# Performance work log

Hardware: AMD Instinct MI355X
Metric: run time of the kernel (lower is better)

## Reference

```python
import jax, jax.numpy as jnp
import numpy as np

N_NODES = 100000
IN_C = 512
HID = 64   # 2 * out_channels
OUT_C = 32
N_EDGES = 2000000  # knn k=20


def gcn_conv(x, src, dst, W, b, n_nodes):
    """PyG GCNConv: symmetric norm with self-loops. Aggregates src -> dst."""
    h = x @ W  # [N, F_out] -- transform first (F_out small)
    ones = jnp.ones(src.shape[0], dtype=h.dtype)
    deg = jax.ops.segment_sum(ones, dst, num_segments=n_nodes) + 1.0  # +1 self-loop
    dinv = jax.lax.rsqrt(deg)  # deg > 0 always due to self-loop
    norm = dinv[src] * dinv[dst]                      # [E]
    msg = h[src] * norm[:, None]                      # gather + scale
    agg = jax.ops.segment_sum(msg, dst, num_segments=n_nodes)
    agg = agg + (dinv * dinv)[:, None] * h            # self-loop contribution
    return agg + b


def setup_inputs() -> dict:
    key = jax.random.key(0)
    ks = jax.random.split(key, 9)
    x = jax.random.normal(ks[0], (N_NODES, IN_C), dtype=jnp.float32)
    edge_index = jax.random.randint(ks[1], (2, N_EDGES), 0, N_NODES, dtype=jnp.int64)
    s1 = 1.0 / np.sqrt(IN_C)
    s2 = 1.0 / np.sqrt(HID)
    W1 = jax.random.uniform(ks[2], (IN_C, HID), jnp.float32, -s1, s1)
    b1 = jnp.zeros((HID,), jnp.float32)
    W_mu = jax.random.uniform(ks[3], (HID, OUT_C), jnp.float32, -s2, s2)
    b_mu = jnp.zeros((OUT_C,), jnp.float32)
    W_ls = jax.random.uniform(ks[4], (HID, OUT_C), jnp.float32, -s2, s2)
    b_ls = jnp.zeros((OUT_C,), jnp.float32)
    return {"x": x, "edge_index": edge_index, "W1": W1, "b1": b1,
            "W_mu": W_mu, "b_mu": b_mu, "W_ls": W_ls, "b_ls": b_ls}


def reference(x, edge_index, W1, b1, W_mu, b_mu, W_ls, b_ls):
    src, dst = edge_index[0], edge_index[1]  # source_to_target flow
    h = jax.nn.relu(gcn_conv(x, src, dst, W1, b1, N_NODES))
    mu = gcn_conv(h, src, dst, W_mu, b_mu, N_NODES)
    logstd = gcn_conv(h, src, dst, W_ls, b_ls, N_NODES)
    return (mu, logstd)
```

## Files before the change

kernel.cpp:

```cpp
#include <hip/hip_runtime.h>
#include <cstdint>
#include <cstddef>

#define MN 100000
#define NE 2000000
#define BSH 7
#define BKN 128
#define NB  782
#define CAP 3072
#define EPB 8192

typedef short bf16x8 __attribute__((ext_vector_type(8)));
typedef float f32x4  __attribute__((ext_vector_type(4)));
typedef unsigned short u16x4 __attribute__((ext_vector_type(4)));

__device__ inline unsigned short f2bf(float f) {
    unsigned int u = __float_as_uint(f);
    unsigned int r = (u + 0x7fffu + ((u >> 16) & 1u)) >> 16;
    return (unsigned short)r;
}
__device__ inline float bf2f(unsigned short h) {
    return __uint_as_float((unsigned int)h << 16);
}

__global__ __launch_bounds__(1024) void bin_kernel(const int* __restrict__ src,
                                                   const int* __restrict__ dst,
                                                   int* __restrict__ gcur,
                                                   unsigned int* __restrict__ binned,
                                                   int nE) {
    __shared__ int hist[NB];
    __shared__ int base[NB];
    const int tid = threadIdx.x;
    const int e0 = blockIdx.x * EPB;
    const int e1 = min(e0 + EPB, nE);

    for (int i = tid; i < NB; i += 1024) hist[i] = 0;
    __syncthreads();
    for (int e = e0 + tid * 4; e < e1; e += 4096) {
        if (e + 4 <= e1) {
            int4 d4 = *reinterpret_cast<const int4*>(dst + e);
            atomicAdd(&hist[d4.x >> BSH], 1);
            atomicAdd(&hist[d4.y >> BSH], 1);
            atomicAdd(&hist[d4.z >> BSH], 1);
            atomicAdd(&hist[d4.w >> BSH], 1);
        } else {
            for (int k = e; k < e1; ++k) atomicAdd(&hist[dst[k] >> BSH], 1);
        }
    }
    __syncthreads();
    for (int i = tid; i < NB; i += 1024) {
        int h = hist[i];
        base[i] = (h > 0) ? atomicAdd(&gcur[i], h) : 0;
        hist[i] = 0;
    }
    __syncthreads();
    for (int e = e0 + tid * 4; e < e1; e += 4096) {
        if (e + 4 <= e1) {
            int4 d4 = *reinterpret_cast<const int4*>(dst + e);
            int4 s4 = *reinterpret_cast<const int4*>(src + e);
            int dd[4] = {d4.x, d4.y, d4.z, d4.w};
            int ss[4] = {s4.x, s4.y, s4.z, s4.w};
#pragma unroll
            for (int k = 0; k < 4; ++k) {
                int b = dd[k] >> BSH;
                int p = base[b] + atomicAdd(&hist[b], 1);
                if (p < CAP)
                    binned[(size_t)b * CAP + p] =
                        ((unsigned int)ss[k] << BSH) | (unsigned int)(dd[k] & (BKN - 1));
            }
        } else {
            for (int k = e; k < e1; ++k) {
                int d = dst[k];
                int b = d >> BSH;
                int p = base[b] + atomicAdd(&hist[b], 1);
                if (p < CAP)
                    binned[(size_t)b * CAP + p] =
                        ((unsigned int)src[k] << BSH) | (unsigned int)(d & (BKN - 1));
            }
        }
    }
}

__global__ __launch_bounds__(1024) void bucket_scan(const int* __restrict__ gcur,
                                                    int* __restrict__ bbase) {
    __shared__ int wsum[16];
    const int lane = threadIdx.x & 63, wid = threadIdx.x >> 6;
    const int i = threadIdx.x;
    int v = (i < NB) ? min(gcur[i], CAP) : 0;
    int x = v;
#pragma unroll
    for (int off = 1; off < 64; off <<= 1) {
        int t = __shfl_up(x, off);
        if (lane >= off) x += t;
    }
    if (lane == 63) wsum[wid] = x;
    __syncthreads();
    if (wid == 0) {
        int w = (lane < 16) ? wsum[lane] : 0;
#pragma unroll
        for (int off = 1; off < 16; off <<= 1) {
            int t = __shfl_up(w, off);
            if (lane >= off) w += t;
        }
        if (lane < 16) wsum[lane] = w;
    }
    __syncthreads();
    int waveoff = (wid > 0) ? wsum[wid - 1] : 0;
    int excl = waveoff + x - v;
    if (i <= NB) bbase[i] = excl;
}

__global__ __launch_bounds__(256) void csr_build(const unsigned int* __restrict__ binned,
                                                 const int* __restrict__ gcur,
                                                 const int* __restrict__ bbase,
                                                 int* __restrict__ rowptr,
                                                 float* __restrict__ dinv,
                                                 int* __restrict__ csr, int M) {
    __shared__ int cnt[BKN];
    __shared__ int pre[BKN];
    __shared__ int cur[BKN];
    const int tid = threadIdx.x, b = blockIdx.x;
    const unsigned int* seg = binned + (size_t)b * CAP;
    const int n = min(gcur[b], CAP);

    if (tid < BKN) cnt[tid] = 0;
    __syncthreads();
    for (int i = tid; i < n; i += 256)
        atomicAdd(&cnt[seg[i] & (BKN - 1)], 1);
    __syncthreads();
    if (tid < BKN) pre[tid] = cnt[tid];
    __syncthreads();
#pragma unroll
    for (int off = 1; off < BKN; off <<= 1) {
        int t = 0;
        if (tid < BKN && tid >= off) t = pre[tid - off];
        __syncthreads();
        if (tid < BKN) pre[tid] += t;
        __syncthreads();
    }
    const int node0 = b << BSH;
    if (tid < BKN) {
        int g = bbase[b] + pre[tid] - cnt[tid];
        cur[tid] = g;
        int node = node0 + tid;
        if (node <= M) rowptr[node] = g;
        if (node < M)  dinv[node] = rsqrtf((float)cnt[tid] + 1.0f);
    }
    __syncthreads();
    for (int i = tid; i < n; i += 256) {
        unsigned int pk = seg[i];
        int p = atomicAdd(&cur[pk & (BKN - 1)], 1);
        csr[p] = (int)(pk >> BSH);
    }
}

__global__ __launch_bounds__(256) void gemm1_mfma(const float* __restrict__ x,
                                                  const float* __restrict__ W,
                                                  const float* __restrict__ dinv,
                                                  unsigned short* __restrict__ out, int M) {
    __shared__ __align__(16) unsigned short Ah[2048], Al[2048], Bh[2048], Bl[2048];
    const int tid  = threadIdx.x;
    const int bm   = blockIdx.x * 64;
    const int wid  = tid >> 6;
    const int lane = tid & 63;
    const int r0   = (wid >> 1) * 2;
    const int c0   = (wid & 1) * 2;

    const int arow = tid >> 2, ag = tid & 3;
    const int bcol = tid & 63, bg = tid >> 6;
    const int achunk_w = ((arow >> 4) * 4 + ag) * 16 + (arow & 15);
    const int bchunk_w = ((bcol >> 4) * 4 + bg) * 16 + (bcol & 15);
    const bool arow_ok = (bm + arow) < M;
    const float* aptr = x + (size_t)(bm + arow) * 512 + ag * 8;

    f32x4 acc[2][2];
#pragma unroll
    for (int i = 0; i < 2; ++i)
#pragma unroll
        for (int j = 0; j < 2; ++j)
#pragma unroll
            for (int r = 0; r < 4; ++r) acc[i][j][r] = 0.f;

    for (int k0 = 0; k0 < 512; k0 += 32) {
        float av[8];
        if (arow_ok) {
            float4 p0 = *reinterpret_cast<const float4*>(aptr + k0);
            float4 p1 = *reinterpret_cast<const float4*>(aptr + k0 + 4);
            av[0] = p0.x; av[1] = p0.y; av[2] = p0.z; av[3] = p0.w;
            av[4] = p1.x; av[5] = p1.y; av[6] = p1.z; av[7] = p1.w;
        } else {
#pragma unroll
            for (int j = 0; j < 8; ++j) av[j] = 0.f;
        }
        union { unsigned short u[8]; int4 v; } ahp, alp;
#pragma unroll
        for (int j = 0; j < 8; ++j) {
            unsigned short h = f2bf(av[j]);
            ahp.u[j] = h;
            alp.u[j] = f2bf(av[j] - bf2f(h));
        }
        *reinterpret_cast<int4*>(&Ah[achunk_w * 8]) = ahp.v;
        *reinterpret_cast<int4*>(&Al[achunk_w * 8]) = alp.v;

        union { unsigned short u[8]; int4 v; } bhp, blp;
#pragma unroll
        for (int j = 0; j < 8; ++j) {
            float wv = W[(size_t)(k0 + bg * 8 + j) * 64 + bcol];
            unsigned short h = f2bf(wv);
            bhp.u[j] = h;
            blp.u[j] = f2bf(wv - bf2f(h));
        }
        *reinterpret_cast<int4*>(&Bh[bchunk_w * 8]) = bhp.v;
        *reinterpret_cast<int4*>(&Bl[bchunk_w * 8]) = blp.v;

        __syncthreads();

        bf16x8 ah[2], al[2], bh[2], bl[2];
#pragma unroll
        for (int rt = 0; rt < 2; ++rt) {
            int ch = ((r0 + rt) * 4 + (lane >> 4)) * 16 + (lane & 15);
            ah[rt] = *reinterpret_cast<const bf16x8*>(&Ah[ch * 8]);
            al[rt] = *reinterpret_cast<const bf16x8*>(&Al[ch * 8]);
        }
#pragma unroll
        for (int ct = 0; ct < 2; ++ct) {
            int ch = ((c0 + ct) * 4 + (lane >> 4)) * 16 + (lane & 15);
            bh[ct] = *reinterpret_cast<const bf16x8*>(&Bh[ch * 8]);
            bl[ct] = *reinterpret_cast<const bf16x8*>(&Bl[ch * 8]);
        }
#pragma unroll
        for (int rt = 0; rt < 2; ++rt)
#pragma unroll
            for (int ct = 0; ct < 2; ++ct) {
                acc[rt][ct] = __builtin_amdgcn_mfma_f32_16x16x32_bf16(ah[rt], bh[ct], acc[rt][ct], 0, 0, 0);
                acc[rt][ct] = __builtin_amdgcn_mfma_f32_16x16x32_bf16(ah[rt], bl[ct], acc[rt][ct], 0, 0, 0);
                acc[rt][ct] = __builtin_amdgcn_mfma_f32_16x16x32_bf16(al[rt], bh[ct], acc[rt][ct], 0, 0, 0);
            }
        __syncthreads();
    }

#pragma unroll
    for (int rt = 0; rt < 2; ++rt) {
#pragma unroll
        for (int reg = 0; reg < 4; ++reg) {
            int irow = (lane >> 4) * 4 + reg;
            int node = bm + (r0 + rt) * 16 + irow;
            if (node < M) {
                float di = dinv[node];
#pragma unroll
                for (int ct = 0; ct < 2; ++ct)
                    out[(size_t)node * 64 + (c0 + ct) * 16 + (lane & 15)] = f2bf(acc[rt][ct][reg] * di);
            }
        }
    }
}

__global__ __launch_bounds__(256) void agg1_kernel(const unsigned short* __restrict__ hs1,
                                                   const int* __restrict__ rowptr,
                                                   const int* __restrict__ csr,
                                                   const float* __restrict__ dinv,
                                                   const float* __restrict__ b1,
                                                   unsigned short* __restrict__ hs2, int M) {
    const int lane = threadIdx.x & 63;
    const int g = lane >> 4, q = lane & 15;
    const int node = blockIdx.x * 4 + (threadIdx.x >> 6);
    if (node >= M) return;
    const int st = rowptr[node], en = rowptr[node + 1];
    const size_t qo = (size_t)q * 4;
    float4 acc = make_float4(0.f, 0.f, 0.f, 0.f);
    int i = st;
    for (; i + 8 <= en; i += 8) {
        int sa = csr[i + g];
        int sb = csr[i + 4 + g];
        u16x4 va = *reinterpret_cast<const u16x4*>(hs1 + (size_t)sa * 64 + qo);
        u16x4 vb = *reinterpret_cast<const u16x4*>(hs1 + (size_t)sb * 64 + qo);
        acc.x += bf2f(va[0]) + bf2f(vb[0]);
        acc.y += bf2f(va[1]) + bf2f(vb[1]);
        acc.z += bf2f(va[2]) + bf2f(vb[2]);
        acc.w += bf2f(va[3]) + bf2f(vb[3]);
    }
    for (; i < en; i += 4) {
        int e = i + g;
        if (e < en) {
            int s = csr[e];
            u16x4 v = *reinterpret_cast<const u16x4*>(hs1 + (size_t)s * 64 + qo);
            acc.x += bf2f(v[0]); acc.y += bf2f(v[1]);
            acc.z += bf2f(v[2]); acc.w += bf2f(v[3]);
        }
    }
#pragma unroll
    for (int m = 16; m <= 32; m <<= 1) {
        acc.x += __shfl_xor(acc.x, m);
        acc.y += __shfl_xor(acc.y, m);
        acc.z += __shfl_xor(acc.z, m);
        acc.w += __shfl_xor(acc.w, m);
    }
    if (g == 0) {
        u16x4 sv = *reinterpret_cast<const u16x4*>(hs1 + (size_t)node * 64 + qo);
        float di = dinv[node];
        float4 bb = *reinterpret_cast<const float4*>(b1 + qo);
        u16x4 hv;
        hv[0] = f2bf(fmaxf(di * (acc.x + bf2f(sv[0])) + bb.x, 0.f) * di);
        hv[1] = f2bf(fmaxf(di * (acc.y + bf2f(sv[1])) + bb.y, 0.f) * di);
        hv[2] = f2bf(fmaxf(di * (acc.z + bf2f(sv[2])) + bb.z, 0.f) * di);
        hv[3] = f2bf(fmaxf(di * (acc.w + bf2f(sv[3])) + bb.w, 0.f) * di);
        *reinterpret_cast<u16x4*>(hs2 + (size_t)node * 64 + qo) = hv;
    }
}

__global__ __launch_bounds__(256) void agg2_fused(const unsigned short* __restrict__ hs2,
                                                  const int* __restrict__ rowptr,
                                                  const int* __restrict__ csr,
                                                  const float* __restrict__ dinv,
                                                  const float* __restrict__ Wmu,
                                                  const float* __restrict__ bmu,
                                                  const float* __restrict__ Wls,
                                                  const float* __restrict__ bls,
                                                  float* __restrict__ out, int M) {
    __shared__ float Wc[64][64];
    __shared__ float rowbuf[4][64];
    const int tid = threadIdx.x;
    const int lane = tid & 63;
    const int wid = tid >> 6;
    const int g = lane >> 4, q = lane & 15;
    const size_t qo = (size_t)q * 4;

    for (int t = tid; t < 4096; t += 256) {
        int k = t >> 6, c = t & 63;
        Wc[k][c] = (c < 32) ? Wmu[k * 32 + c] : Wls[k * 32 + (c - 32)];
    }
    __syncthreads();

    const float bval = (lane < 32) ? bmu[lane] : bls[lane - 32];
    const int node0 = blockIdx.x * 32;

    for (int r = 0; r < 8; ++r) {
        const int node = node0 + wid * 8 + r;
        if (node >= M) break;
        const int st = rowptr[node], en = rowptr[node + 1];
        float4 acc = make_float4(0.f, 0.f, 0.f, 0.f);
        int i = st;
        for (; i + 8 <= en; i += 8) {
            int sa = csr[i + g];
            int sb = csr[i + 4 + g];
            u16x4 va = *reinterpret_cast<const u16x4*>(hs2 + (size_t)sa * 64 + qo);
            u16x4 vb = *reinterpret_cast<const u16x4*>(hs2 + (size_t)sb * 64 + qo);
            acc.x += bf2f(va[0]) + bf2f(vb[0]);
            acc.y += bf2f(va[1]) + bf2f(vb[1]);
            acc.z += bf2f(va[2]) + bf2f(vb[2]);
            acc.w += bf2f(va[3]) + bf2f(vb[3]);
        }
        for (; i < en; i += 4) {
            int e = i + g;
            if (e < en) {
                int s = csr[e];
                u16x4 v = *reinterpret_cast<const u16x4*>(hs2 + (size_t)s * 64 + qo);
                acc.x += bf2f(v[0]); acc.y += bf2f(v[1]);
                acc.z += bf2f(v[2]); acc.w += bf2f(v[3]);
            }
        }
#pragma unroll
        for (int m = 16; m <= 32; m <<= 1) {
            acc.x += __shfl_xor(acc.x, m);
            acc.y += __shfl_xor(acc.y, m);
            acc.z += __shfl_xor(acc.z, m);
            acc.w += __shfl_xor(acc.w, m);
        }
        if (g == 0) {
            u16x4 sv = *reinterpret_cast<const u16x4*>(hs2 + (size_t)node * 64 + qo);
            float di = dinv[node];
            float4 av;
            av.x = di * (acc.x + bf2f(sv[0]));
            av.y = di * (acc.y + bf2f(sv[1]));
            av.z = di * (acc.z + bf2f(sv[2]));
            av.w = di * (acc.w + bf2f(sv[3]));
            *reinterpret_cast<float4*>(&rowbuf[wid][q * 4]) = av;
        }
        float o = 0.f;
        const float* rb = rowbuf[wid];
#pragma unroll 4
        for (int k = 0; k < 64; ++k)
            o += rb[k] * Wc[k][lane];
        if (lane < 32)
            out[(size_t)node * 32 + lane] = o + bval;
        else
            out[(size_t)MN * 32 + (size_t)node * 32 + (lane - 32)] = o + bval;
    }
}

extern "C" void kernel_launch(void* const* d_in, const int* in_sizes, int n_in,
                              void* d_out, int out_size, void* d_ws, size_t ws_size,
                              hipStream_t stream) {
    const float* x   = (const float*)d_in[0];
    const int*   ei  = (const int*)d_in[1];
    const float* W1  = (const float*)d_in[2];
    const float* b1  = (const float*)d_in[3];
    const float* Wmu = (const float*)d_in[4];
    const float* bmu = (const float*)d_in[5];
    const float* Wls = (const float*)d_in[6];
    const float* bls = (const float*)d_in[7];
    float* out = (float*)d_out;

    const int M = MN, E = NE;
    const int* src = ei;
    const int* dst = ei + E;

    const size_t bf_feat_bytes = (size_t)M * 64 * sizeof(unsigned short);
    char* w = (char*)d_ws;
    size_t off = 0;
    auto alloc = [&](size_t bytes) {
        char* p = w + off;
        off = (off + bytes + 255) & ~(size_t)255;
        return p;
    };
    int*            gcur   = (int*)           alloc((size_t)NB * 4);
    int*            bbase  = (int*)           alloc((size_t)(NB + 1) * 4);
    unsigned int*   binned = (unsigned int*)  alloc((size_t)NB * CAP * 4);
    int*            rowptr = (int*)           alloc((size_t)(M + 1) * 4);
    int*            csr    = (int*)           alloc((size_t)E * 4);
    float*          dinv   = (float*)         alloc((size_t)M * 4);
    unsigned short* hs1    = (unsigned short*)alloc(bf_feat_bytes);
    unsigned short* hs2    = (unsigned short*)alloc(bf_feat_bytes);

    hipMemsetAsync(gcur, 0, (size_t)NB * 4, stream);

    bin_kernel<<<(E + EPB - 1) / EPB, 1024, 0, stream>>>(src, dst, gcur, binned, E);
    bucket_scan<<<1, 1024, 0, stream>>>(gcur, bbase);
    csr_build<<<NB, 256, 0, stream>>>(binned, gcur, bbase, rowptr, dinv, csr, M);

    gemm1_mfma<<<(M + 63) / 64, 256, 0, stream>>>(x, W1, dinv, hs1, M);
    agg1_kernel<<<(M + 3) / 4, 256, 0, stream>>>(hs1, rowptr, csr, dinv, b1, hs2, M);
    agg2_fused<<<(M + 31) / 32, 256, 0, stream>>>(hs2, rowptr, csr, dinv, Wmu, bmu, Wls, bls, out, M);
}
```

Measured before the change: 251.6 us.

## Precompute split-bf16 W1, drop bucket scan, restructure GEMM and widen gathers

A small kernel now converts W1 into hi/lo bf16 once, in the MFMA fragment layout. The GEMM then reads B fragments directly from global memory with no LDS staging or barriers, and each wave computes 16 rows by 64 columns. The global bucket scan is removed by giving each bucket a fixed CAP-sized CSR segment, with per-node start and end arrays in place of a single rowptr. The aggregation kernels gather 8 bf16 per lane (16-byte loads) across 8 edge groups instead of 4. The risk is redundant global B reads per wave in the GEMM and a larger, padded CSR array.

```diff
diff --git a/kernel.cpp b/kernel.cpp
--- a/kernel.cpp
+++ b/kernel.cpp
@@ -12,7 +12,7 @@
 
 typedef short bf16x8 __attribute__((ext_vector_type(8)));
 typedef float f32x4  __attribute__((ext_vector_type(4)));
-typedef unsigned short u16x4 __attribute__((ext_vector_type(4)));
+typedef unsigned short u16x8 __attribute__((ext_vector_type(8)));
 
 __device__ inline unsigned short f2bf(float f) {
     unsigned int u = __float_as_uint(f);
@@ -21,6 +21,24 @@
 }
 __device__ inline float bf2f(unsigned short h) {
     return __uint_as_float((unsigned int)h << 16);
+}
+
+__global__ __launch_bounds__(256) void w1_convert(const float* __restrict__ W,
+                                                  unsigned short* __restrict__ Whi,
+                                                  unsigned short* __restrict__ Wlo) {
+    const int t = blockIdx.x * 256 + threadIdx.x;
+    const int col = t & 63;
+    const int kb  = (t >> 6) * 8;
+    union { unsigned short u[8]; int4 v; } hp, lp;
+#pragma unroll
+    for (int j = 0; j < 8; ++j) {
+        float wv = W[(size_t)(kb + j) * 64 + col];
+        unsigned short hh = f2bf(wv);
+        hp.u[j] = hh;
+        lp.u[j] = f2bf(wv - bf2f(hh));
+    }
+    *reinterpret_cast<int4*>(Whi + (size_t)t * 8) = hp.v;
+    *reinterpret_cast<int4*>(Wlo + (size_t)t * 8) = lp.v;
 }
 
 __global__ __launch_bounds__(1024) void bin_kernel(const int* __restrict__ src,
@@ -81,39 +99,10 @@
     }
 }
 
-__global__ __launch_bounds__(1024) void bucket_scan(const int* __restrict__ gcur,
-                                                    int* __restrict__ bbase) {
-    __shared__ int wsum[16];
-    const int lane = threadIdx.x & 63, wid = threadIdx.x >> 6;
-    const int i = threadIdx.x;
-    int v = (i < NB) ? min(gcur[i], CAP) : 0;
-    int x = v;
-#pragma unroll
-    for (int off = 1; off < 64; off <<= 1) {
-        int t = __shfl_up(x, off);
-        if (lane >= off) x += t;
-    }
-    if (lane == 63) wsum[wid] = x;
-    __syncthreads();
-    if (wid == 0) {
-        int w = (lane < 16) ? wsum[lane] : 0;
-#pragma unroll
-        for (int off = 1; off < 16; off <<= 1) {
-            int t = __shfl_up(w, off);
-            if (lane >= off) w += t;
-        }
-        if (lane < 16) wsum[lane] = w;
-    }
-    __syncthreads();
-    int waveoff = (wid > 0) ? wsum[wid - 1] : 0;
-    int excl = waveoff + x - v;
-    if (i <= NB) bbase[i] = excl;
-}
-
 __global__ __launch_bounds__(256) void csr_build(const unsigned int* __restrict__ binned,
                                                  const int* __restrict__ gcur,
-                                                 const int* __restrict__ bbase,
                                                  int* __restrict__ rowptr,
+                                                 int* __restrict__ rowend,
                                                  float* __restrict__ dinv,
                                                  int* __restrict__ csr, int M) {
     __shared__ int cnt[BKN];
@@ -140,11 +129,14 @@
     }
     const int node0 = b << BSH;
     if (tid < BKN) {
-        int g = bbase[b] + pre[tid] - cnt[tid];
+        int g = b * CAP + pre[tid] - cnt[tid];
         cur[tid] = g;
         int node = node0 + tid;
-        if (node <= M) rowptr[node] = g;
-        if (node < M)  dinv[node] = rsqrtf((float)cnt[tid] + 1.0f);
+        if (node < M) {
+            rowptr[node] = g;
+            rowend[node] = g + cnt[tid];
+            dinv[node] = rsqrtf((float)cnt[tid] + 1.0f);
+        }
     }
     __syncthreads();
     for (int i = tid; i < n; i += 256) {
@@ -155,161 +147,123 @@
 }
 
 __global__ __launch_bounds__(256) void gemm1_mfma(const float* __restrict__ x,
-                                                  const float* __restrict__ W,
+                                                  const unsigned short* __restrict__ Whi,
+                                                  const unsigned short* __restrict__ Wlo,
                                                   const float* __restrict__ dinv,
                                                   unsigned short* __restrict__ out, int M) {
-    __shared__ __align__(16) unsigned short Ah[2048], Al[2048], Bh[2048], Bl[2048];
     const int tid  = threadIdx.x;
+    const int lane = tid & 63;
+    const int wid  = tid >> 6;
     const int bm   = blockIdx.x * 64;
-    const int wid  = tid >> 6;
-    const int lane = tid & 63;
-    const int r0   = (wid >> 1) * 2;
-    const int c0   = (wid & 1) * 2;
-
-    const int arow = tid >> 2, ag = tid & 3;
-    const int bcol = tid & 63, bg = tid >> 6;
-    const int achunk_w = ((arow >> 4) * 4 + ag) * 16 + (arow & 15);
-    const int bchunk_w = ((bcol >> 4) * 4 + bg) * 16 + (bcol & 15);
-    const bool arow_ok = (bm + arow) < M;
-    const float* aptr = x + (size_t)(bm + arow) * 512 + ag * 8;
-
-    f32x4 acc[2][2];
-#pragma unroll
-    for (int i = 0; i < 2; ++i)
-#pragma unroll
-        for (int j = 0; j < 2; ++j)
-#pragma unroll
-            for (int r = 0; r < 4; ++r) acc[i][j][r] = 0.f;
-
-    for (int k0 = 0; k0 < 512; k0 += 32) {
+    const int kg   = lane >> 4;
+    const int rlo  = lane & 15;
+    const int arow = bm + wid * 16 + rlo;
+    const bool rok = arow < M;
+    const float* aptr = x + (size_t)arow * 512 + kg * 8;
+
+    f32x4 acc[4];
+#pragma unroll
+    for (int c = 0; c < 4; ++c)
+#pragma unroll
+        for (int r = 0; r < 4; ++r) acc[c][r] = 0.f;
+
+    for (int s = 0; s < 16; ++s) {
         float av[8];
-        if (arow_ok) {
-            float4 p0 = *reinterpret_cast<const float4*>(aptr + k0);
-            float4 p1 = *reinterpret_cast<const float4*>(aptr + k0 + 4);
+        if (rok) {
+            float4 p0 = *reinterpret_cast<const float4*>(aptr + s * 32);
+            float4 p1 = *reinterpret_cast<const float4*>(aptr + s * 32 + 4);
             av[0] = p0.x; av[1] = p0.y; av[2] = p0.z; av[3] = p0.w;
             av[4] = p1.x; av[5] = p1.y; av[6] = p1.z; av[7] = p1.w;
         } else {
 #pragma unroll
             for (int j = 0; j < 8; ++j) av[j] = 0.f;
         }
-        union { unsigned short u[8]; int4 v; } ahp, alp;
+        union { unsigned short u[8]; bf16x8 v; } ah, al;
 #pragma unroll
         for (int j = 0; j < 8; ++j) {
             unsigned short h = f2bf(av[j]);
-            ahp.u[j] = h;
-            alp.u[j] = f2bf(av[j] - bf2f(h));
-        }
-        *reinterpret_cast<int4*>(&Ah[achunk_w * 8]) = ahp.v;
-        *reinterpret_cast<int4*>(&Al[achunk_w * 8]) = alp.v;
-
-        union { unsigned short u[8]; int4 v; } bhp, blp;
-#pragma unroll
-        for (int j = 0; j < 8; ++j) {
-            float wv = W[(size_t)(k0 + bg * 8 + j) * 64 + bcol];
-            unsigned short h = f2bf(wv);
-            bhp.u[j] = h;
-            blp.u[j] = f2bf(wv - bf2f(h));
-        }
-        *reinterpret_cast<int4*>(&Bh[bchunk_w * 8]) = bhp.v;
-        *reinterpret_cast<int4*>(&Bl[bchunk_w * 8]) = blp.v;
-
-        __syncthreads();
-
-        bf16x8 ah[2], al[2], bh[2], bl[2];
-#pragma unroll
-        for (int rt = 0; rt < 2; ++rt) {
-            int ch = ((r0 + rt) * 4 + (lane >> 4)) * 16 + (lane & 15);
-            ah[rt] = *reinterpret_cast<const bf16x8*>(&Ah[ch * 8]);
-            al[rt] = *reinterpret_cast<const bf16x8*>(&Al[ch * 8]);
-        }
-#pragma unroll
-        for (int ct = 0; ct < 2; ++ct) {
-            int ch = ((c0 + ct) * 4 + (lane >> 4)) * 16 + (lane & 15);
-            bh[ct] = *reinterpret_cast<const bf16x8*>(&Bh[ch * 8]);
-            bl[ct] = *reinterpret_cast<const bf16x8*>(&Bl[ch * 8]);
-        }
-#pragma unroll
-        for (int rt = 0; rt < 2; ++rt)
-#pragma unroll
-            for (int ct = 0; ct < 2; ++ct) {
-                acc[rt][ct] = __builtin_amdgcn_mfma_f32_16x16x32_bf16(ah[rt], bh[ct], acc[rt][ct], 0, 0, 0);
-                acc[rt][ct] = __builtin_amdgcn_mfma_f32_16x16x32_bf16(ah[rt], bl[ct], acc[rt][ct], 0, 0, 0);
-                acc[rt][ct] = __builtin_amdgcn_mfma_f32_16x16x32_bf16(al[rt], bh[ct], acc[rt][ct], 0, 0, 0);
-            }
-        __syncthreads();
-    }
-
-#pragma unroll
-    for (int rt = 0; rt < 2; ++rt) {
-#pragma unroll
-        for (int reg = 0; reg < 4; ++reg) {
-            int irow = (lane >> 4) * 4 + reg;
-            int node = bm + (r0 + rt) * 16 + irow;
-            if (node < M) {
-                float di = dinv[node];
-#pragma unroll
-                for (int ct = 0; ct < 2; ++ct)
-                    out[(size_t)node * 64 + (c0 + ct) * 16 + (lane & 15)] = f2bf(acc[rt][ct][reg] * di);
-            }
+            ah.u[j] = h;
+            al.u[j] = f2bf(av[j] - bf2f(h));
+        }
+        const size_t cb = ((size_t)((s * 4 + kg) * 64 + rlo)) * 8;
+#pragma unroll
+        for (int c = 0; c < 4; ++c) {
+            bf16x8 bh = *reinterpret_cast<const bf16x8*>(Whi + cb + (size_t)c * 16 * 8);
+            bf16x8 bl = *reinterpret_cast<const bf16x8*>(Wlo + cb + (size_t)c * 16 * 8);
+            acc[c] = __builtin_amdgcn_mfma_f32_16x16x32_bf16(ah.v, bh, acc[c], 0, 0, 0);
+            acc[c] = __builtin_amdgcn_mfma_f32_16x16x32_bf16(al.v, bh, acc[c], 0, 0, 0);
+            acc[c] = __builtin_amdgcn_mfma_f32_16x16x32_bf16(ah.v, bl, acc[c], 0, 0, 0);
+        }
+    }
+
+#pragma unroll
+    for (int reg = 0; reg < 4; ++reg) {
+        int node = bm + wid * 16 + kg * 4 + reg;
+        if (node < M) {
+            float di = dinv[node];
+#pragma unroll
+            for (int c = 0; c < 4; ++c)
+                out[(size_t)node * 64 + c * 16 + rlo] = f2bf(acc[c][reg] * di);
         }
     }
 }
 
 __global__ __launch_bounds__(256) void agg1_kernel(const unsigned short* __restrict__ hs1,
                                                    const int* __restrict__ rowptr,
+                                                   const int* __restrict__ rowend,
                                                    const int* __restrict__ csr,
                                                    const float* __restrict__ dinv,
                                                    const float* __restrict__ b1,
                                                    unsigned short* __restrict__ hs2, int M) {
     const int lane = threadIdx.x & 63;
-    const int g = lane >> 4, q = lane & 15;
+    const int g = lane >> 3, q = lane & 7;
     const int node = blockIdx.x * 4 + (threadIdx.x >> 6);
     if (node >= M) return;
-    const int st = rowptr[node], en = rowptr[node + 1];
-    const size_t qo = (size_t)q * 4;
-    float4 acc = make_float4(0.f, 0.f, 0.f, 0.f);
+    const int st = rowptr[node], en = rowend[node];
+    const size_t qo = (size_t)q * 8;
+    float a[8];
+#pragma unroll
+    for (int j = 0; j < 8; ++j) a[j] = 0.f;
     int i = st;
-    for (; i + 8 <= en; i += 8) {
+    for (; i + 16 <= en; i += 16) {
         int sa = csr[i + g];
-        int sb = csr[i + 4 + g];
-        u16x4 va = *reinterpret_cast<const u16x4*>(hs1 + (size_t)sa * 64 + qo);
-        u16x4 vb = *reinterpret_cast<const u16x4*>(hs1 + (size_t)sb * 64 + qo);
-        acc.x += bf2f(va[0]) + bf2f(vb[0]);
-        acc.y += bf2f(va[1]) + bf2f(vb[1]);
-        acc.z += bf2f(va[2]) + bf2f(vb[2]);
-        acc.w += bf2f(va[3]) + bf2f(vb[3]);
-    }
-    for (; i < en; i += 4) {
+        int sb = csr[i + 8 + g];
+        u16x8 va = *reinterpret_cast<const u16x8*>(hs1 + (size_t)sa * 64 + qo);
+        u16x8 vb = *reinterpret_cast<const u16x8*>(hs1 + (size_t)sb * 64 + qo);
+#pragma unroll
+        for (int j = 0; j < 8; ++j) a[j] += bf2f(va[j]) + bf2f(vb[j]);
+    }
+    for (; i < en; i += 8) {
         int e = i + g;
         if (e < en) {
             int s = csr[e];
-            u16x4 v = *reinterpret_cast<const u16x4*>(hs1 + (size_t)s * 64 + qo);
-            acc.x += bf2f(v[0]); acc.y += bf2f(v[1]);
-            acc.z += bf2f(v[2]); acc.w += bf2f(v[3]);
-        }
-    }
-#pragma unroll
-    for (int m = 16; m <= 32; m <<= 1) {
-        acc.x += __shfl_xor(acc.x, m);
-        acc.y += __shfl_xor(acc.y, m);
-        acc.z += __shfl_xor(acc.z, m);
-        acc.w += __shfl_xor(acc.w, m);
-    }
+            u16x8 v = *reinterpret_cast<const u16x8*>(hs1 + (size_t)s * 64 + qo);
+#pragma unroll
+            for (int j = 0; j < 8; ++j) a[j] += bf2f(v[j]);
+        }
+    }
+#pragma unroll
+    for (int m = 8; m <= 32; m <<= 1)
+#pragma unroll
+        for (int j = 0; j < 8; ++j) a[j] += __shfl_xor(a[j], m);
+
     if (g == 0) {
-        u16x4 sv = *reinterpret_cast<const u16x4*>(hs1 + (size_t)node * 64 + qo);
+        u16x8 sv = *reinterpret_cast<const u16x8*>(hs1 + (size_t)node * 64 + qo);
         float di = dinv[node];
-        float4 bb = *reinterpret_cast<const float4*>(b1 + qo);
-        u16x4 hv;
-        hv[0] = f2bf(fmaxf(di * (acc.x + bf2f(sv[0])) + bb.x, 0.f) * di);
-        hv[1] = f2bf(fmaxf(di * (acc.y + bf2f(sv[1])) + bb.y, 0.f) * di);
-        hv[2] = f2bf(fmaxf(di * (acc.z + bf2f(sv[2])) + bb.z, 0.f) * di);
-        hv[3] = f2bf(fmaxf(di * (acc.w + bf2f(sv[3])) + bb.w, 0.f) * di);
-        *reinterpret_cast<u16x4*>(hs2 + (size_t)node * 64 + qo) = hv;
+        float4 b0 = *reinterpret_cast<const float4*>(b1 + qo);
+        float4 b4 = *reinterpret_cast<const float4*>(b1 + qo + 4);
+        float bb[8] = {b0.x, b0.y, b0.z, b0.w, b4.x, b4.y, b4.z, b4.w};
+        u16x8 hv;
+#pragma unroll
+        for (int j = 0; j < 8; ++j)
+            hv[j] = f2bf(fmaxf(di * (a[j] + bf2f(sv[j])) + bb[j], 0.f) * di);
+        *reinterpret_cast<u16x8*>(hs2 + (size_t)node * 64 + qo) = hv;
     }
 }
 
 __global__ __launch_bounds__(256) void agg2_fused(const unsigned short* __restrict__ hs2,
                                                   const int* __restrict__ rowptr,
+                                                  const int* __restrict__ rowend,
                                                   const int* __restrict__ csr,
                                                   const float* __restrict__ dinv,
                                                   const float* __restrict__ Wmu,
@@ -322,8 +276,8 @@
     const int tid = threadIdx.x;
     const int lane = tid & 63;
     const int wid = tid >> 6;
-    const int g = lane >> 4, q = lane & 15;
-    const size_t qo = (size_t)q * 4;
+    const int g = lane >> 3, q = lane & 7;
+    const size_t qo = (size_t)q * 8;
 
     for (int t = tid; t < 4096; t += 256) {
         int k = t >> 6, c = t & 63;
@@ -337,44 +291,47 @@
     for (int r = 0; r < 8; ++r) {
         const int node = node0 + wid * 8 + r;
         if (node >= M) break;
-        const int st = rowptr[node], en = rowptr[node + 1];
-        float4 acc = make_float4(0.f, 0.f, 0.f, 0.f);
+        const int st = rowptr[node], en = rowend[node];
+        float a[8];
+#pragma unroll
+        for (int j = 0; j < 8; ++j) a[j] = 0.f;
         int i = st;
-        for (; i + 8 <= en; i += 8) {
+        for (; i + 16 <= en; i += 16) {
             int sa = csr[i + g];
-            int sb = csr[i + 4 + g];
-            u16x4 va = *reinterpret_cast<const u16x4*>(hs2 + (size_t)sa * 64 + qo);
-            u16x4 vb = *reinterpret_cast<const u16x4*>(hs2 + (size_t)sb * 64 + qo);
-            acc.x += bf2f(va[0]) + bf2f(vb[0]);
-            acc.y += bf2f(va[1]) + bf2f(vb[1]);
-            acc.z += bf2f(va[2]) + bf2f(vb[2]);
-            acc.w += bf2f(va[3]) + bf2f(vb[3]);
-        }
-        for (; i < en; i += 4) {
+            int sb = csr[i + 8 + g];
+            u16x8 va = *reinterpret_cast<const u16x8*>(hs2 + (size_t)sa * 64 + qo);
+            u16x8 vb = *reinterpret_cast<const u16x8*>(hs2 + (size_t)sb * 64 + qo);
+#pragma unroll
+            for (int j = 0; j < 8; ++j) a[j] += bf2f(va[j]) + bf2f(vb[j]);
+        }
+        for (; i < en; i += 8) {
             int e = i + g;
             if (e < en) {
                 int s = csr[e];
-                u16x4 v = *reinterpret_cast<const u16x4*>(hs2 + (size_t)s * 64 + qo);
-                acc.x += bf2f(v[0]); acc.y += bf2f(v[1]);
-                acc.z += bf2f(v[2]); acc.w += bf2f(v[3]);
+                u16x8 v = *reinterpret_cast<const u16x8*>(hs2 + (size_t)s * 64 + qo);
+#pragma unroll
+                for (int j = 0; j < 8; ++j) a[j] += bf2f(v[j]);
             }
         }
 #pragma unroll
-        for (int m = 16; m <= 32; m <<= 1) {
-            acc.x += __shfl_xor(acc.x, m);
-            acc.y += __shfl_xor(acc.y, m);
-            acc.z += __shfl_xor(acc.z, m);
-            acc.w += __shfl_xor(acc.w, m);
-        }
+        for (int m = 8; m <= 32; m <<= 1)
+#pragma unroll
+            for (int j = 0; j < 8; ++j) a[j] += __shfl_xor(a[j], m);
+
         if (g == 0) {
-            u16x4 sv = *reinterpret_cast<const u16x4*>(hs2 + (size_t)node * 64 + qo);
+            u16x8 sv = *reinterpret_cast<const u16x8*>(hs2 + (size_t)node * 64 + qo);
             float di = dinv[node];
-            float4 av;
-            av.x = di * (acc.x + bf2f(sv[0]));
-            av.y = di * (acc.y + bf2f(sv[1]));
-            av.z = di * (acc.z + bf2f(sv[2]));
-            av.w = di * (acc.w + bf2f(sv[3]));
-            *reinterpret_cast<float4*>(&rowbuf[wid][q * 4]) = av;
+            float4 lo, hi;
+            lo.x = di * (a[0] + bf2f(sv[0]));
+            lo.y = di * (a[1] + bf2f(sv[1]));
+            lo.z = di * (a[2] + bf2f(sv[2]));
+            lo.w = di * (a[3] + bf2f(sv[3]));
+            hi.x = di * (a[4] + bf2f(sv[4]));
+            hi.y = di * (a[5] + bf2f(sv[5]));
+            hi.z = di * (a[6] + bf2f(sv[6]));
+            hi.w = di * (a[7] + bf2f(sv[7]));
+            *reinterpret_cast<float4*>(&rowbuf[wid][q * 8]) = lo;
+            *reinterpret_cast<float4*>(&rowbuf[wid][q * 8 + 4]) = hi;
         }
         float o = 0.f;
         const float* rb = rowbuf[wid];
@@ -414,21 +371,24 @@
         return p;
     };
     int*            gcur   = (int*)           alloc((size_t)NB * 4);
-    int*            bbase  = (int*)           alloc((size_t)(NB + 1) * 4);
     unsigned int*   binned = (unsigned int*)  alloc((size_t)NB * CAP * 4);
-    int*            rowptr = (int*)           alloc((size_t)(M + 1) * 4);
-    int*            csr    = (int*)           alloc((size_t)E * 4);
+    int*            rowptr = (int*)           alloc((size_t)M * 4);
+    int*            rowend = (int*)           alloc((size_t)M * 4);
+    int*            csr    = (int*)           alloc((size_t)NB * CAP * 4);
     float*          dinv   = (float*)         alloc((size_t)M * 4);
+    unsigned short* Whi    = (unsigned short*)alloc((size_t)512 * 64 * 2);
+    unsigned short* Wlo    = (unsigned short*)alloc((size_t)512 * 64 * 2);
     unsigned short* hs1    = (unsigned short*)alloc(bf_feat_bytes);
     unsigned short* hs2    = (unsigned short*)alloc(bf_feat_bytes);
 
     hipMemsetAsync(gcur, 0, (size_t)NB * 4, stream);
 
+    w1_convert<<<16, 256, 0, stream>>>(W1, Whi, Wlo);
     bin_kernel<<<(E + EPB - 1) / EPB, 1024, 0, stream>>>(src, dst, gcur, binned, E);
-    bucket_scan<<<1, 1024, 0, stream>>>(gcur, bbase);
-    csr_build<<<NB, 256, 0, stream>>>(binned, gcur, bbase, rowptr, dinv, csr, M);
-
-    gemm1_mfma<<<(M + 63) / 64, 256, 0, stream>>>(x, W1, dinv, hs1, M);
-    agg1_kernel<<<(M + 3) / 4, 256, 0, stream>>>(hs1, rowptr, csr, dinv, b1, hs2, M);
-    agg2_fused<<<(M + 31) / 32, 256, 0, stream>>>(hs2, rowptr, csr, dinv, Wmu, bmu, Wls, bls, out, M);
-}
+    csr_build<<<NB, 256, 0, stream>>>(binned, gcur, rowptr, rowend, dinv, csr, M);
+
+    gemm1_mfma<<<(M + 63) / 64, 256, 0, stream>>>(x, Whi, Wlo, dinv, hs1, M);
+    agg1_kernel<<<(M + 3) / 4, 256, 0, stream>>>(hs1, rowptr, rowend, csr, dinv, b1, hs2, M);
+    agg2_fused<<<(M + 31) / 32, 256, 0, stream>>>(hs2, rowptr, rowend, csr, dinv,
+                                                  Wmu, bmu, Wls, bls, out, M);
+}
```

Measured after the change: 242.9 us. 1.04x faster.
